# Optimization experiments

Measured on AMD Instinct MI355X. Metric: run time of the kernel, lower is better.

Reference implementation:

```python
import jax, jax.numpy as jnp
import numpy as np


def _gcn_conv(x, src, dst, W, b, num_nodes, deg_inv_sqrt):
    # PyG GCNConv: h = x @ W, then normalized scatter-add over edges (incl. self loops), + bias
    h = x @ W  # [N, d_out]
    norm = deg_inv_sqrt[src] * deg_inv_sqrt[dst]  # [E']
    msg = h[src] * norm[:, None]  # gather + scale, [E', d_out]
    out = jax.ops.segment_sum(msg, dst, num_segments=num_nodes)  # scatter-add to targets
    return out + b


def reference(x, edge_index, W1, b1, W2, b2, num_nodes):
    src0, dst0 = edge_index[0], edge_index[1]
    loop = jnp.arange(num_nodes, dtype=edge_index.dtype)
    # add self loops (PyG default add_self_loops=True)
    src = jnp.concatenate([src0, loop])
    dst = jnp.concatenate([dst0, loop])
    # symmetric normalization D^{-1/2} (A+I) D^{-1/2}, degree from self-looped graph
    deg = jax.ops.segment_sum(jnp.ones_like(src, dtype=x.dtype), dst, num_segments=num_nodes)
    deg_inv_sqrt = jnp.where(deg > 0, jax.lax.rsqrt(jnp.maximum(deg, 1)), 0.0).astype(x.dtype)

    z = jax.nn.relu(_gcn_conv(x, src, dst, W1, b1, num_nodes, deg_inv_sqrt))
    z = jax.nn.relu(_gcn_conv(z, src, dst, W2, b2, num_nodes, deg_inv_sqrt))
    return z


def setup_inputs() -> dict:
    key = jax.random.key(0)
    k1, k2, k3, k4 = jax.random.split(key, 4)
    N, E, D, H = 50000, 1600000, 128, 128
    x = jax.random.normal(k1, (N, D), dtype=jnp.float32)
    edge_index = jax.random.randint(k2, (2, E), 0, N, dtype=jnp.int64)
    s = 1.0 / np.sqrt(D)
    W1 = jax.random.normal(k3, (D, H), dtype=jnp.float32) * s
    W2 = jax.random.normal(k4, (H, H), dtype=jnp.float32) * s
    return {
        "x": x,
        "edge_index": edge_index,
        "W1": W1,
        "b1": jnp.zeros((H,), jnp.float32),
        "W2": W2,
        "b2": jnp.zeros((H,), jnp.float32),
        "num_nodes": N,
    }
```

## Files before the change

### kernel.cpp

```cpp
#include <hip/hip_runtime.h>

#define FD 128
#define BSH 7
#define CH 2048
#define CHT 8
#define KMAX 512
#define SCAP 8192

typedef __attribute__((ext_vector_type(8))) short bf16x8;
typedef __attribute__((ext_vector_type(4))) float f32x4;

__device__ inline unsigned bfr(float f) {
    unsigned u = __float_as_uint(f);
    return (u + 0x7FFF + ((u >> 16) & 1)) >> 16;
}
__device__ inline float uplo(unsigned p) { return __uint_as_float(p << 16); }
__device__ inline float uphi(unsigned p) { return __uint_as_float(p & 0xFFFF0000u); }


__global__ __launch_bounds__(256) void partition_kernel(
        const int* __restrict__ src, const int* __restrict__ dst,
        int* __restrict__ lstartG, int* __restrict__ total,
        int* __restrict__ pairs, int E, int K) {
    __shared__ int lcnt[KMAX];
    __shared__ int lstart[KMAX];
    __shared__ int sm[256];
    __shared__ int staged[CH];
    int t = threadIdx.x;
    int base = blockIdx.x * CH;
    int n = min(CH, E - base);

    lcnt[t] = 0; lcnt[t + 256] = 0;
    __syncthreads();

    int pk[CHT]; int bn[CHT];
    #pragma unroll
    for (int j = 0; j < CHT; ++j) {
        int i = t + j * 256;
        bn[j] = -1;
        if (i < n) {
            int d = dst[base + i];
            int s = src[base + i];
            bn[j] = d >> BSH;
            pk[j] = ((d & ((1 << BSH) - 1)) << 17) | s;
            atomicAdd(&lcnt[bn[j]], 1);
        }
    }
    __syncthreads();

    int c0 = lcnt[2 * t], c1 = lcnt[2 * t + 1];
    int s2 = c0 + c1;
    sm[t] = s2;
    __syncthreads();
    for (int off = 1; off < 256; off <<= 1) {
        int add = (t >= off) ? sm[t - off] : 0;
        __syncthreads();
        sm[t] += add;
        __syncthreads();
    }
    int ex = sm[t] - s2;
    lstart[2 * t] = ex;     lstart[2 * t + 1] = ex + c0;
    lcnt[2 * t]   = ex;     lcnt[2 * t + 1]   = ex + c0;
    __syncthreads();

    #pragma unroll
    for (int j = 0; j < CHT; ++j) {
        if (bn[j] >= 0) {
            int pos = atomicAdd(&lcnt[bn[j]], 1);
            staged[pos] = pk[j];
        }
    }
    __syncthreads();

    for (int i = t; i < n; i += 256)
        pairs[base + i] = staged[i];

    size_t lrow = (size_t)blockIdx.x * (K + 1);
    for (int b = t; b < K; b += 256) {
        lstartG[lrow + b] = lstart[b];
        int c = lcnt[b] - lstart[b];
        if (c) atomicAdd(&total[b], c);
    }
    if (t == 0) lstartG[lrow + K] = n;
}

__global__ __launch_bounds__(512) void totscan_kernel(
        const int* __restrict__ total, int* __restrict__ bbase,
        int* __restrict__ rp, int K, int E, int N) {
    __shared__ int sm[512];
    int t = threadIdx.x;
    int v = (t < K) ? total[t] : 0;
    sm[t] = v;
    __syncthreads();
    for (int off = 1; off < 512; off <<= 1) {
        int add = (t >= off) ? sm[t - off] : 0;
        __syncthreads();
        sm[t] += add;
        __syncthreads();
    }
    if (t < K) bbase[t] = sm[t] - v;
    if (t == 0) { bbase[K] = E; rp[N] = E; }
}

__global__ __launch_bounds__(256) void build_kernel(
        const int* __restrict__ pairs, const int* __restrict__ lstartG,
        const int* __restrict__ bbase, int* __restrict__ rp,
        float* __restrict__ dis, int* __restrict__ col, int N, int PB, int K) {
    __shared__ int staged[SCAP];
    __shared__ int lcnt[1 << BSH];
    __shared__ int lsum[1 << BSH];
    __shared__ int lbase[1 << BSH];
    __shared__ int sm[256];
    int b = blockIdx.x;
    int t = threadIdx.x;
    int nbase = b << BSH;
    int nn = min(1 << BSH, N - nbase);
    int beg = bbase[b];
    int cnt = bbase[b + 1] - beg;

    int fp[4], fl0[4], flen[4];
    int nf = 0, mysum = 0;
    for (int p = t; p < PB; p += 256) {
        size_t lrow = (size_t)p * (K + 1);
        int l0 = lstartG[lrow + b];
        int l1 = lstartG[lrow + b + 1];
        fp[nf] = p; fl0[nf] = l0; flen[nf] = l1 - l0;
        mysum += l1 - l0;
        ++nf;
    }
    sm[t] = mysum;
    __syncthreads();
    for (int off = 1; off < 256; off <<= 1) {
        int add = (t >= off) ? sm[t - off] : 0;
        __syncthreads();
        sm[t] += add;
        __syncthreads();
    }
    int o = sm[t] - mysum;

    if (t < 128) lcnt[t] = 0;

    if (cnt <= SCAP) {
        for (int f = 0; f < nf; ++f) {
            int gbase = fp[f] * CH + fl0[f];
            for (int i = 0; i < flen[f]; ++i) staged[o + i] = pairs[gbase + i];
            o += flen[f];
        }
        __syncthreads();
        for (int i = t; i < cnt; i += 256) atomicAdd(&lcnt[staged[i] >> 17], 1);
    } else {
        __syncthreads();
        for (int f = 0; f < nf; ++f) {
            int gbase = fp[f] * CH + fl0[f];
            for (int i = 0; i < flen[f]; ++i)
                atomicAdd(&lcnt[pairs[gbase + i] >> 17], 1);
        }
    }
    __syncthreads();

    if (t < 128) lsum[t] = lcnt[t];
    __syncthreads();
    for (int off = 1; off < 128; off <<= 1) {
        int add = (t < 128 && t >= off) ? lsum[t - off] : 0;
        __syncthreads();
        if (t < 128) lsum[t] += add;
        __syncthreads();
    }
    if (t < 128) {
        int excl = beg + lsum[t] - lcnt[t];
        lbase[t] = excl;
        if (t < nn) {
            rp[nbase + t] = excl;
            dis[nbase + t] = rsqrtf((float)(lcnt[t] + 1));
        }
    }
    __syncthreads();
    if (t < 128) lcnt[t] = lbase[t];
    __syncthreads();

    if (cnt <= SCAP) {
        for (int i = t; i < cnt; i += 256) {
            int p = staged[i];
            int pos = atomicAdd(&lcnt[p >> 17], 1);
            col[pos] = p & 0x1FFFF;
        }
    } else {
        for (int f = 0; f < nf; ++f) {
            int gbase = fp[f] * CH + fl0[f];
            for (int i = 0; i < flen[f]; ++i) {
                int p = pairs[gbase + i];
                int pos = atomicAdd(&lcnt[p >> 17], 1);
                col[pos] = p & 0x1FFFF;
            }
        }
    }
}


__global__ void wt_kernel(const float* __restrict__ W1, unsigned short* __restrict__ W1T,
                          const float* __restrict__ W2, unsigned short* __restrict__ W2T) {
    int k = blockIdx.x & (FD - 1);
    int n = threadIdx.x;
    if (blockIdx.x < FD) W1T[n * FD + k] = (unsigned short)bfr(W1[k * FD + n]);
    else                 W2T[n * FD + k] = (unsigned short)bfr(W2[k * FD + n]);
}


#define APAD 8
#define ASTR (FD + APAD)

template <bool A32>
__device__ void gemm_body(const void* __restrict__ Ap,
                          const unsigned short* __restrict__ WT,
                          const float* __restrict__ dis,
                          unsigned short* __restrict__ C, int M) {
    __shared__ unsigned short Bs[128 * ASTR];
    int tid = threadIdx.x;
    int lane = tid & 63;
    int wave = tid >> 6;
    int quad = lane >> 4;
    int l16 = lane & 15;
    int rowBase = blockIdx.x * 128;

    #pragma unroll
    for (int p = 0; p < 8; ++p) {
        int r = p * 16 + (tid >> 4);
        int cq = (tid & 15) * 8;
        *(uint4*)&Bs[r * ASTR + cq] = *(const uint4*)&WT[(size_t)r * FD + cq];
    }
    __syncthreads();

    int m0 = wave * 32;
    int r0 = rowBase + m0 + l16;
    int r1 = r0 + 16;
    f32x4 acc[2][8] = {};
    #pragma unroll
    for (int kt = 0; kt < 4; ++kt) {
        int ko = kt * 32 + quad * 8;
        uint4 va = make_uint4(0u, 0u, 0u, 0u);
        uint4 vb = make_uint4(0u, 0u, 0u, 0u);
        if (A32) {
            const float* A = (const float*)Ap;
            if (r0 < M) {
                const float* a = A + (size_t)r0 * FD + ko;
                float4 f0 = *(const float4*)a;
                float4 f1 = *(const float4*)(a + 4);
                va.x = bfr(f0.x) | (bfr(f0.y) << 16);
                va.y = bfr(f0.z) | (bfr(f0.w) << 16);
                va.z = bfr(f1.x) | (bfr(f1.y) << 16);
                va.w = bfr(f1.z) | (bfr(f1.w) << 16);
            }
            if (r1 < M) {
                const float* a = A + (size_t)r1 * FD + ko;
                float4 f0 = *(const float4*)a;
                float4 f1 = *(const float4*)(a + 4);
                vb.x = bfr(f0.x) | (bfr(f0.y) << 16);
                vb.y = bfr(f0.z) | (bfr(f0.w) << 16);
                vb.z = bfr(f1.x) | (bfr(f1.y) << 16);
                vb.w = bfr(f1.z) | (bfr(f1.w) << 16);
            }
        } else {
            const unsigned short* A = (const unsigned short*)Ap;
            if (r0 < M) va = *(const uint4*)(A + (size_t)r0 * FD + ko);
            if (r1 < M) vb = *(const uint4*)(A + (size_t)r1 * FD + ko);
        }
        bf16x8 a0 = *(bf16x8*)&va;
        bf16x8 a1 = *(bf16x8*)&vb;
        #pragma unroll
        for (int n = 0; n < 8; ++n) {
            bf16x8 b = *(bf16x8*)&Bs[(n * 16 + l16) * ASTR + ko];
            acc[0][n] = __builtin_amdgcn_mfma_f32_16x16x32_bf16(a0, b, acc[0][n], 0, 0, 0);
            acc[1][n] = __builtin_amdgcn_mfma_f32_16x16x32_bf16(a1, b, acc[1][n], 0, 0, 0);
        }
    }

    #pragma unroll
    for (int ms = 0; ms < 2; ++ms) {
        #pragma unroll
        for (int r = 0; r < 4; ++r) {
            int grow = rowBase + m0 + ms * 16 + quad * 4 + r;
            if (grow < M) {
                float dv = dis[grow];
                #pragma unroll
                for (int n = 0; n < 8; ++n) {
                    C[(size_t)grow * FD + n * 16 + l16] =
                        (unsigned short)bfr(dv * acc[ms][n][r]);
                }
            }
        }
    }
}

__global__ __launch_bounds__(256) void gemm_mfma_f32(
        const float* __restrict__ A, const unsigned short* __restrict__ WT,
        const float* __restrict__ dis, unsigned short* __restrict__ C, int M) {
    gemm_body<true>(A, WT, dis, C, M);
}

__global__ __launch_bounds__(256) void gemm_mfma_bf16(
        const unsigned short* __restrict__ A, const unsigned short* __restrict__ WT,
        const float* __restrict__ dis, unsigned short* __restrict__ C, int M) {
    gemm_body<false>(A, WT, dis, C, M);
}


__global__ __launch_bounds__(256) void agg_kernel(
        const unsigned* __restrict__ h, const float* __restrict__ dis,
        const int* __restrict__ rp, const int* __restrict__ col,
        const float2* __restrict__ bias, void* __restrict__ out, int N, int obf) {
    int v = blockIdx.x * 4 + threadIdx.y;
    v = __builtin_amdgcn_readfirstlane(v);
    if (v >= N) return;
    int t = threadIdx.x;
    float dv = dis[v];
    size_t vb = (size_t)v * 64 + t;
    unsigned hp = h[vb];
    float2 acc;
    acc.x = uplo(hp); acc.y = uphi(hp);
    int e = rp[v];
    int end = rp[v + 1];

    for (; e + 16 <= end; e += 16) {
        int u[16];
        #pragma unroll
        for (int j = 0; j < 16; ++j) u[j] = col[e + j];
        unsigned p[16];
        #pragma unroll
        for (int j = 0; j < 16; ++j) p[j] = h[(size_t)u[j] * 64 + t];
        #pragma unroll
        for (int j = 0; j < 16; ++j) {
            acc.x += uplo(p[j]); acc.y += uphi(p[j]);
        }
    }
    for (; e + 4 <= end; e += 4) {
        int u0 = col[e], u1 = col[e + 1], u2 = col[e + 2], u3 = col[e + 3];
        unsigned p0 = h[(size_t)u0 * 64 + t];
        unsigned p1 = h[(size_t)u1 * 64 + t];
        unsigned p2 = h[(size_t)u2 * 64 + t];
        unsigned p3 = h[(size_t)u3 * 64 + t];
        acc.x += uplo(p0); acc.y += uphi(p0);
        acc.x += uplo(p1); acc.y += uphi(p1);
        acc.x += uplo(p2); acc.y += uphi(p2);
        acc.x += uplo(p3); acc.y += uphi(p3);
    }
    for (; e < end; ++e) {
        unsigned p = h[(size_t)col[e] * 64 + t];
        acc.x += uplo(p); acc.y += uphi(p);
    }

    float2 bb = bias[t];
    float2 r;
    r.x = fmaxf(fmaf(dv, acc.x, bb.x), 0.0f);
    r.y = fmaxf(fmaf(dv, acc.y, bb.y), 0.0f);
    if (obf) {
        ((unsigned*)out)[vb] = bfr(r.x) | (bfr(r.y) << 16);
    } else {
        ((float2*)out)[vb] = r;
    }
}


extern "C" void kernel_launch(void* const* d_in, const int* in_sizes, int n_in,
                              void* d_out, int out_size, void* d_ws, size_t ws_size,
                              hipStream_t stream) {
    const float* x  = (const float*)d_in[0];
    const int*   ei = (const int*)d_in[1];
    const float* W1 = (const float*)d_in[2];
    const float* b1 = (const float*)d_in[3];
    const float* W2 = (const float*)d_in[4];
    const float* b2 = (const float*)d_in[5];

    int N = in_sizes[0] / FD;
    int E = in_sizes[1] / 2;
    const int* src = ei;
    const int* dst = ei + E;
    int K = (N + (1 << BSH) - 1) >> BSH;
    int PB = (E + CH - 1) / CH;

    char* base = (char*)d_ws;
    size_t off = 0;
    auto align256 = [](size_t v) { return (v + 255) & ~(size_t)255; };
    int*            rp    = (int*)(base + off);            off += align256((size_t)(N + 1) * 4);
    float*          dis   = (float*)(base + off);          off += align256((size_t)N * 4);
    int*            total = (int*)(base + off);            off += align256(512 * 4);
    int*            bbase = (int*)(base + off);            off += align256(513 * 4);
    unsigned short* w1t   = (unsigned short*)(base + off); off += align256((size_t)FD * FD * 2);
    unsigned short* w2t   = (unsigned short*)(base + off); off += align256((size_t)FD * FD * 2);
    int*            col   = (int*)(base + off);            off += align256((size_t)E * 4);
    unsigned short* hbuf  = (unsigned short*)(base + off); off += align256((size_t)N * FD * 2);
    unsigned short* z1    = (unsigned short*)(base + off); off += align256((size_t)N * FD * 2);
    int*            pairs = (int*)(base + off);            off += align256((size_t)E * 4);
    int*            lstartG = (int*)hbuf;
    (void)ws_size; (void)n_in; (void)out_size;

    (void)hipMemsetAsync(total, 0, 512 * 4, stream);
    partition_kernel<<<PB, 256, 0, stream>>>(src, dst, lstartG, total, pairs, E, K);
    totscan_kernel  <<<1, 512, 0, stream>>>(total, bbase, rp, K, E, N);
    build_kernel    <<<K, 256, 0, stream>>>(pairs, lstartG, bbase, rp, dis, col, N, PB, K);

    wt_kernel<<<2 * FD, FD, 0, stream>>>(W1, w1t, W2, w2t);

    dim3 aggBlk(64, 4);
    int aggGrid = (N + 3) / 4;
    int gemmGrid = (N + 127) / 128;

    gemm_mfma_f32 <<<gemmGrid, 256, 0, stream>>>(x, w1t, dis, hbuf, N);
    agg_kernel<<<aggGrid, aggBlk, 0, stream>>>((const unsigned*)hbuf, dis, rp, col,
                                               (const float2*)b1, z1, N, 1);
    gemm_mfma_bf16<<<gemmGrid, 256, 0, stream>>>(z1, w2t, dis, hbuf, N);
    agg_kernel<<<aggGrid, aggBlk, 0, stream>>>((const unsigned*)hbuf, dis, rp, col,
                                               (const float2*)b2, d_out, N, 0);
}
```

Before: 257.0 us.

## Transpose partition offsets, double chunk size, and per-wave counters in CSR build

Adds a tiled transpose kernel so build_kernel reads per-bucket chunk offsets contiguously instead of with a stride of K+1. The partition chunk size is doubled, which halves the number of chunks the build kernel walks. Node counters are split four ways by wavefront to cut LDS atomic contention, and the counting pass is fused into the staging loop. This adds an extra kernel launch and a 512-entry scan. Scatter order now follows each thread's own chunk rather than a strided sweep, so column order within a row changes.

```diff
diff --git a/kernel.cpp b/kernel.cpp
--- a/kernel.cpp
+++ b/kernel.cpp
@@ -2,8 +2,8 @@
 
 #define FD 128
 #define BSH 7
-#define CH 2048
-#define CHT 8
+#define CH 4096
+#define CHT 16
 #define KMAX 512
 #define SCAP 8192
 
@@ -102,28 +102,43 @@
     if (t == 0) { bbase[K] = E; rp[N] = E; }
 }
 
+__global__ __launch_bounds__(256) void tr_kernel(
+        const int* __restrict__ A, int* __restrict__ B, int R, int C) {
+    __shared__ int tile[32][33];
+    int c0 = blockIdx.x * 32, r0 = blockIdx.y * 32;
+    int tx = threadIdx.x, ty = threadIdx.y;
+    for (int i = ty; i < 32; i += 8) {
+        int r = r0 + i, c = c0 + tx;
+        if (r < R && c < C) tile[i][tx] = A[(size_t)r * C + c];
+    }
+    __syncthreads();
+    for (int i = ty; i < 32; i += 8) {
+        int c = c0 + i, r = r0 + tx;
+        if (c < C && r < R) B[(size_t)c * R + r] = tile[tx][i];
+    }
+}
+
 __global__ __launch_bounds__(256) void build_kernel(
-        const int* __restrict__ pairs, const int* __restrict__ lstartG,
+        const int* __restrict__ pairs, const int* __restrict__ lstartT,
         const int* __restrict__ bbase, int* __restrict__ rp,
         float* __restrict__ dis, int* __restrict__ col, int N, int PB, int K) {
     __shared__ int staged[SCAP];
-    __shared__ int lcnt[1 << BSH];
-    __shared__ int lsum[1 << BSH];
-    __shared__ int lbase[1 << BSH];
+    __shared__ int lcnt[512];
+    __shared__ int pref[512];
     __shared__ int sm[256];
     int b = blockIdx.x;
     int t = threadIdx.x;
+    int wv = t >> 6;
     int nbase = b << BSH;
     int nn = min(1 << BSH, N - nbase);
     int beg = bbase[b];
     int cnt = bbase[b + 1] - beg;
 
-    int fp[4], fl0[4], flen[4];
+    int fp[2], fl0[2], flen[2];
     int nf = 0, mysum = 0;
     for (int p = t; p < PB; p += 256) {
-        size_t lrow = (size_t)p * (K + 1);
-        int l0 = lstartG[lrow + b];
-        int l1 = lstartG[lrow + b + 1];
+        int l0 = lstartT[(size_t)b * PB + p];
+        int l1 = lstartT[(size_t)(b + 1) * PB + p];
         fp[nf] = p; fl0[nf] = l0; flen[nf] = l1 - l0;
         mysum += l1 - l0;
         ++nf;
@@ -138,58 +153,69 @@
     }
     int o = sm[t] - mysum;
 
-    if (t < 128) lcnt[t] = 0;
+    lcnt[t] = 0; lcnt[t + 256] = 0;
+    __syncthreads();
 
     if (cnt <= SCAP) {
+        int oo = o;
         for (int f = 0; f < nf; ++f) {
             int gbase = fp[f] * CH + fl0[f];
-            for (int i = 0; i < flen[f]; ++i) staged[o + i] = pairs[gbase + i];
-            o += flen[f];
-        }
-        __syncthreads();
-        for (int i = t; i < cnt; i += 256) atomicAdd(&lcnt[staged[i] >> 17], 1);
+            for (int i = 0; i < flen[f]; ++i) {
+                int p = pairs[gbase + i];
+                staged[oo + i] = p;
+                atomicAdd(&lcnt[((p >> 17) << 2) | wv], 1);
+            }
+            oo += flen[f];
+        }
     } else {
-        __syncthreads();
         for (int f = 0; f < nf; ++f) {
             int gbase = fp[f] * CH + fl0[f];
             for (int i = 0; i < flen[f]; ++i)
-                atomicAdd(&lcnt[pairs[gbase + i] >> 17], 1);
-        }
-    }
-    __syncthreads();
-
-    if (t < 128) lsum[t] = lcnt[t];
-    __syncthreads();
-    for (int off = 1; off < 128; off <<= 1) {
-        int add = (t < 128 && t >= off) ? lsum[t - off] : 0;
-        __syncthreads();
-        if (t < 128) lsum[t] += add;
-        __syncthreads();
-    }
-    if (t < 128) {
-        int excl = beg + lsum[t] - lcnt[t];
-        lbase[t] = excl;
-        if (t < nn) {
-            rp[nbase + t] = excl;
-            dis[nbase + t] = rsqrtf((float)(lcnt[t] + 1));
-        }
-    }
-    __syncthreads();
-    if (t < 128) lcnt[t] = lbase[t];
+                atomicAdd(&lcnt[((pairs[gbase + i] >> 17) << 2) | wv], 1);
+        }
+    }
+    __syncthreads();
+
+    int c0 = lcnt[2 * t], c1 = lcnt[2 * t + 1];
+    int s2 = c0 + c1;
+    sm[t] = s2;
+    __syncthreads();
+    for (int off = 1; off < 256; off <<= 1) {
+        int add = (t >= off) ? sm[t - off] : 0;
+        __syncthreads();
+        sm[t] += add;
+        __syncthreads();
+    }
+    int ex = sm[t] - s2;
+    pref[2 * t] = ex;  pref[2 * t + 1] = ex + c0;
+    __syncthreads();
+
+    if (t < 128 && t < nn) {
+        int rs = pref[t << 2];
+        int re = (t < 127) ? pref[(t + 1) << 2] : cnt;
+        rp[nbase + t] = beg + rs;
+        dis[nbase + t] = rsqrtf((float)(re - rs + 1));
+    }
+    lcnt[2 * t]     = beg + pref[2 * t];
+    lcnt[2 * t + 1] = beg + pref[2 * t + 1];
     __syncthreads();
 
     if (cnt <= SCAP) {
-        for (int i = t; i < cnt; i += 256) {
-            int p = staged[i];
-            int pos = atomicAdd(&lcnt[p >> 17], 1);
-            col[pos] = p & 0x1FFFF;
+        int oo = o;
+        for (int f = 0; f < nf; ++f) {
+            for (int i = 0; i < flen[f]; ++i) {
+                int p = staged[oo + i];
+                int pos = atomicAdd(&lcnt[((p >> 17) << 2) | wv], 1);
+                col[pos] = p & 0x1FFFF;
+            }
+            oo += flen[f];
         }
     } else {
         for (int f = 0; f < nf; ++f) {
             int gbase = fp[f] * CH + fl0[f];
             for (int i = 0; i < flen[f]; ++i) {
                 int p = pairs[gbase + i];
-                int pos = atomicAdd(&lcnt[p >> 17], 1);
+                int pos = atomicAdd(&lcnt[((p >> 17) << 2) | wv], 1);
                 col[pos] = p & 0x1FFFF;
             }
         }
@@ -391,12 +417,16 @@
     unsigned short* z1    = (unsigned short*)(base + off); off += align256((size_t)N * FD * 2);
     int*            pairs = (int*)(base + off);            off += align256((size_t)E * 4);
     int*            lstartG = (int*)hbuf;
+    int*            lstartT = (int*)z1;
     (void)ws_size; (void)n_in; (void)out_size;
 
     (void)hipMemsetAsync(total, 0, 512 * 4, stream);
     partition_kernel<<<PB, 256, 0, stream>>>(src, dst, lstartG, total, pairs, E, K);
     totscan_kernel  <<<1, 512, 0, stream>>>(total, bbase, rp, K, E, N);
-    build_kernel    <<<K, 256, 0, stream>>>(pairs, lstartG, bbase, rp, dis, col, N, PB, K);
+    dim3 trb(32, 8);
+    dim3 trg((K + 1 + 31) / 32, (PB + 31) / 32);
+    tr_kernel       <<<trg, trb, 0, stream>>>(lstartG, lstartT, PB, K + 1);
+    build_kernel    <<<K, 256, 0, stream>>>(pairs, lstartT, bbase, rp, dis, col, N, PB, K);
 
     wt_kernel<<<2 * FD, FD, 0, stream>>>(W1, w1t, W2, w2t);
 
```

Measured after the change: 248.4 us. 1.03x faster.
